# Kernel tuning notes

Hardware: AMD Instinct MI355X
Metric: run time of the kernel (lower is better)

The kernel has to match this reference:

```python
import jax, jax.numpy as jnp
import numpy as np

N = 50000      # nodes
E = 1600000    # edges
F_IN = 128     # input_dim
H = 160        # hidden_dim
G = 512        # graphs in batch
C = 2          # num_classes
EPS = 1e-5     # BatchNorm eps


def setup_inputs() -> dict:
    key = jax.random.key(0)
    ks = jax.random.split(key, 12)
    x = jax.random.normal(ks[0], (N, F_IN), jnp.float32)
    edge_index = jax.random.randint(ks[1], (2, E), 0, N, dtype=jnp.int32)
    batch = jnp.sort(jax.random.randint(ks[2], (N,), 0, G, dtype=jnp.int32))

    def lin(k, fi, fo):
        s = 1.0 / np.sqrt(fi)
        kw, kb = jax.random.split(k)
        W = jax.random.uniform(kw, (fi, fo), jnp.float32, -s, s)
        b = jax.random.uniform(kb, (fo,), jnp.float32, -s, s)
        return W, b

    W1, b1 = lin(ks[3], F_IN, H)
    W2, b2 = lin(ks[4], H, H)
    W3, b3 = lin(ks[5], H, H)
    Wc1, bc1 = lin(ks[6], H, H // 2)
    Wc2, bc2 = lin(ks[7], H // 2, C)

    def bn(k):
        k1, k2, k3, k4 = jax.random.split(k, 4)
        gamma = jax.random.uniform(k1, (H,), jnp.float32, 0.5, 1.5)
        beta = jax.random.normal(k2, (H,), jnp.float32) * 0.1
        mean = jax.random.normal(k3, (H,), jnp.float32) * 0.1
        var = jax.random.uniform(k4, (H,), jnp.float32, 0.5, 1.5)
        return gamma, beta, mean, var

    g1, be1, m1, v1 = bn(ks[8])
    g2, be2, m2, v2 = bn(ks[9])
    g3, be3, m3, v3 = bn(ks[10])

    return dict(x=x, edge_index=edge_index, batch=batch,
                W1=W1, b1=b1, W2=W2, b2=b2, W3=W3, b3=b3,
                g1=g1, be1=be1, m1=m1, v1=v1,
                g2=g2, be2=be2, m2=m2, v2=v2,
                g3=g3, be3=be3, m3=m3, v3=v3,
                Wc1=Wc1, bc1=bc1, Wc2=Wc2, bc2=bc2)


def gcn_conv(x, W, b, src, dst):
    """PyG GCNConv: symmetric deg normalization with self-loops; lin -> aggregate -> +bias."""
    n = x.shape[0]
    h = x @ W                                   # [N, H]
    loop = jnp.arange(n, dtype=src.dtype)
    s = jnp.concatenate([src, loop])            # self-loops appended
    d = jnp.concatenate([dst, loop])
    deg = jax.ops.segment_sum(jnp.ones_like(d, jnp.float32), d, num_segments=n)
    inv = jnp.where(deg > 0, jax.lax.rsqrt(deg), 0.0)
    msg = h[s] * (inv[s] * inv[d])[:, None]     # [E+N, H] gather + norm
    return jax.ops.segment_sum(msg, d, num_segments=n) + b


def bn_eval(x, gamma, beta, mean, var):
    return (x - mean) * jax.lax.rsqrt(var + EPS) * gamma + beta


def reference(x, edge_index, batch, W1, b1, W2, b2, W3, b3,
              g1, be1, m1, v1, g2, be2, m2, v2, g3, be3, m3, v3,
              Wc1, bc1, Wc2, bc2):
    src, dst = edge_index[0], edge_index[1]
    # eval mode: dropout is identity, BN uses running stats
    h = jax.nn.relu(bn_eval(gcn_conv(x, W1, b1, src, dst), g1, be1, m1, v1))
    h = jax.nn.relu(bn_eval(gcn_conv(h, W2, b2, src, dst), g2, be2, m2, v2))
    h = jax.nn.relu(bn_eval(gcn_conv(h, W3, b3, src, dst), g3, be3, m3, v3))
    # global mean pool over graph ids
    sums = jax.ops.segment_sum(h, batch, num_segments=G)
    cnt = jax.ops.segment_sum(jnp.ones((h.shape[0],), jnp.float32), batch, num_segments=G)
    pooled = sums / jnp.clip(cnt, 1.0)[:, None]
    # MLP head
    z = jax.nn.relu(pooled @ Wc1 + bc1)
    return z @ Wc2 + bc2
```

## Files before the change

### kernel.cpp

```cpp
#include <hip/hip_runtime.h>

#define N_NODES   50000
#define N_EDGES   1600000
#define FDIM_IN   128
#define HDIM      160
#define N_GRAPHS  512
#define BN_EPS    1e-5f
#define NBKT_MAX  256
#define BKT_SH    8
#define HIST_BLOCKS 128

typedef _Float16 h2   __attribute__((ext_vector_type(2)));
typedef _Float16 f16x8 __attribute__((ext_vector_type(8)));
typedef float  facc4 __attribute__((ext_vector_type(4)));


__device__ __forceinline__ unsigned short f2h_bits(float f) {
    union { _Float16 h; unsigned short s; } c;
    c.h = (_Float16)f;
    return c.s;
}

__device__ __forceinline__ unsigned int pkh(float lo, float hi) {
    return (unsigned int)f2h_bits(lo) | ((unsigned int)f2h_bits(hi) << 16);
}

__device__ __forceinline__ h2 u2h(unsigned int u) {
    union { unsigned int u; h2 h; } c; c.u = u; return c.h;
}

__device__ __forceinline__ unsigned int h2u(h2 h) {
    union { unsigned int u; h2 h; } c; c.h = h; return c.u;
}

__device__ __forceinline__ void addpk16(h2* acc, uint4 r) {
    acc[0] += u2h(r.x);
    acc[1] += u2h(r.y);
    acc[2] += u2h(r.z);
    acc[3] += u2h(r.w);
}


__global__ __launch_bounds__(256) void coarse_hist_kernel(const int* __restrict__ dst,
                                                          int* __restrict__ cg, int E) {
    __shared__ int h[NBKT_MAX];
    int tid = threadIdx.x;
    if (tid < NBKT_MAX) h[tid] = 0;
    __syncthreads();
    for (int e = blockIdx.x * 256 + tid; e < E; e += gridDim.x * 256)
        atomicAdd(&h[dst[e] >> BKT_SH], 1);
    __syncthreads();
    if (tid < NBKT_MAX) cg[blockIdx.x * NBKT_MAX + tid] = h[tid];
}


struct PrepArgs {
    const float *b, *g, *be, *m, *v;
    float *sc, *sh;
};

__global__ __launch_bounds__(256) void setup_kernel(const int* __restrict__ cg,
                                                    int* __restrict__ bucket_base,
                                                    int* __restrict__ bucket_cursor,
                                                    PrepArgs a0, PrepArgs a1, PrepArgs a2,
                                                    const float* __restrict__ W1,
                                                    const float* __restrict__ W2,
                                                    const float* __restrict__ W3,
                                                    unsigned short* __restrict__ o1,
                                                    unsigned short* __restrict__ o2,
                                                    unsigned short* __restrict__ o3) {
    int bid = blockIdx.x;
    int t = threadIdx.x;
    if (bid == 0) {
        __shared__ int h[NBKT_MAX];
        __shared__ int total;
        if (t < NBKT_MAX) {
            int s = 0;
            for (int b = 0; b < HIST_BLOCKS; ++b) s += cg[b * NBKT_MAX + t];
            h[t] = s;
        }
        __syncthreads();
        if (t == 0) {
            int run = 0;
            for (int i = 0; i < NBKT_MAX; ++i) { int c = h[i]; h[i] = run; run += c; }
            total = run;
        }
        __syncthreads();
        if (t < NBKT_MAX) {
            bucket_base[t] = h[t];
            bucket_cursor[t] = h[t];
        }
        if (t == 0) bucket_base[NBKT_MAX] = total;
    } else if (bid <= 3) {
        PrepArgs a = (bid == 1) ? a0 : (bid == 2) ? a1 : a2;
        if (t < HDIM) {
            float s = a.g[t] * rsqrtf(a.v[t] + BN_EPS);
            a.sc[t] = s;
            a.sh[t] = (a.b[t] - a.m[t]) * s + a.be[t];
        }
    } else {
        int i = (bid - 4) * 256 + t;
        const float* W;
        unsigned short* o;
        if (i < 128 * 160)                 { W = W1; o = o1; }
        else if (i < 128 * 160 + 160 * 160) { W = W2; o = o2; i -= 128 * 160; }
        else if (i < 128 * 160 + 2 * 160 * 160) { W = W3; o = o3; i -= 128 * 160 + 160 * 160; }
        else return;
        int j = i & 7;
        int l = (i >> 3) & 63;
        int u = (i >> 9) % 10;
        int tt = i / 5120;
        int k = tt * 32 + (l >> 4) * 8 + j;
        int nn = u * 16 + (l & 15);
        o[i] = f2h_bits(W[k * 160 + nn]);
    }
}

__global__ __launch_bounds__(256) void part_kernel(const int* __restrict__ src,
                                                   const int* __restrict__ dst,
                                                   int* __restrict__ bucket_cursor,
                                                   unsigned int* __restrict__ pairs, int E) {
    __shared__ int bcnt[NBKT_MAX], bbase[NBKT_MAX], lc[NBKT_MAX];
    int tid = threadIdx.x;
    int per = (E + gridDim.x - 1) / gridDim.x;
    int beg = blockIdx.x * per;
    int end = min(beg + per, E);
    if (tid < NBKT_MAX) { bcnt[tid] = 0; lc[tid] = 0; }
    __syncthreads();
    for (int e = beg + tid; e < end; e += 256)
        atomicAdd(&bcnt[dst[e] >> BKT_SH], 1);
    __syncthreads();
    if (tid < NBKT_MAX)
        bbase[tid] = bcnt[tid] ? atomicAdd(&bucket_cursor[tid], bcnt[tid]) : 0;
    __syncthreads();
    for (int e = beg + tid; e < end; e += 256) {
        int d = dst[e];
        int b = d >> BKT_SH;
        int pos = bbase[b] + atomicAdd(&lc[b], 1);
        pairs[pos] = ((unsigned int)src[e] << BKT_SH) | (unsigned int)(d & (NBKT_MAX - 1));
    }
}

__global__ __launch_bounds__(1024) void bucket_csr_kernel(const unsigned int* __restrict__ pairs,
                                                          const int* __restrict__ bucket_base,
                                                          int* __restrict__ row_off,
                                                          float* __restrict__ inv,
                                                          int* __restrict__ ssrc,
                                                          const float* __restrict__ x,
                                                          unsigned short* __restrict__ xs,
                                                          int n) {
    __shared__ int h[NBKT_MAX];
    __shared__ int ws[4];
    __shared__ float sinv[NBKT_MAX];
    int tid = threadIdx.x;
    int b = blockIdx.x;
    int node0 = b << BKT_SH;
    int beg = bucket_base[b], end = bucket_base[b + 1];
    if (tid < NBKT_MAX) h[tid] = 0;
    __syncthreads();
    for (int j = beg + tid; j < end; j += 1024)
        atomicAdd(&h[pairs[j] & (NBKT_MAX - 1)], 1);
    __syncthreads();
    int cntv = (tid < NBKT_MAX) ? h[tid] : 0;
    __syncthreads();
    int lane = tid & 63, wid = tid >> 6;
    int incl = cntv;
    #pragma unroll
    for (int off = 1; off < 64; off <<= 1) {
        int u = __shfl_up(incl, off);
        if (lane >= off) incl += u;
    }
    if (tid < NBKT_MAX && lane == 63) ws[wid] = incl;
    __syncthreads();
    if (tid == 0) {
        int r = 0;
        #pragma unroll
        for (int i = 0; i < 4; ++i) { int t = ws[i]; ws[i] = r; r += t; }
    }
    __syncthreads();
    int excl = (tid < NBKT_MAX) ? (ws[wid] + incl - cntv) : 0;
    if (tid < NBKT_MAX) {
        float iv = rsqrtf((float)(cntv + 1));
        int node = node0 + tid;
        if (node < n) {
            row_off[node] = beg + excl;
            inv[node] = iv;
        }
        sinv[tid] = iv;
        h[tid] = excl;
    }
    if (tid == 0 && (node0 + NBKT_MAX) >= n) row_off[n] = end;
    __syncthreads();
    for (int j = beg + tid; j < end; j += 1024) {
        unsigned int p = pairs[j];
        int pos = beg + atomicAdd(&h[p & (NBKT_MAX - 1)], 1);
        ssrc[pos] = (int)(p >> BKT_SH);
    }
    for (int idx = tid; idx < NBKT_MAX * 32; idx += 1024) {
        int nd = node0 + (idx >> 5);
        if (nd < n) {
            float w = sinv[idx >> 5];
            float4 v = ((const float4*)x)[(size_t)nd * 32 + (idx & 31)];
            ushort4 o;
            o.x = f2h_bits(v.x * w); o.y = f2h_bits(v.y * w);
            o.z = f2h_bits(v.z * w); o.w = f2h_bits(v.w * w);
            ((ushort4*)xs)[(size_t)nd * 32 + (idx & 31)] = o;
        }
    }
}


template <int C>
__global__ __launch_bounds__(256) void agg_grp_kernel(const unsigned short* __restrict__ in_s,
                                                      const float* __restrict__ inv,
                                                      const int* __restrict__ row_off,
                                                      const int* __restrict__ ssrc,
                                                      unsigned short* __restrict__ out,
                                                      int base, int n) {
    constexpr int LPR = C / 8;
    constexpr int G   = 64 / LPR;
    constexpr int RB  = C * 2;
    int wave = threadIdx.x >> 6;
    int lane = threadIdx.x & 63;
    int node = base + blockIdx.x * 4 + wave;
    if (node >= n) return;
    int g  = lane / LPR;
    int cl = lane - g * LPR;
    bool act = g < G;
    int beg = row_off[node], end = row_off[node + 1];
    const char* bptr = (const char*)in_s;
    int lb = cl * 16;

    h2 acc[4];
    #pragma unroll
    for (int i = 0; i < 4; ++i) acc[i] = (h2){(_Float16)0.f, (_Float16)0.f};

    if (g == 0) {
        uint4 r = *(const uint4*)(bptr + (size_t)node * RB + lb);
        addpk16(acc, r);
    }

    int e = act ? beg + g : end;
    for (; e + G < end; e += 2 * G) {
        int s0 = ssrc[e], s1 = ssrc[e + G];
        uint4 r0 = *(const uint4*)(bptr + (size_t)s0 * RB + lb);
        uint4 r1 = *(const uint4*)(bptr + (size_t)s1 * RB + lb);
        addpk16(acc, r0);
        addpk16(acc, r1);
    }
    if (e < end) {
        uint4 r = *(const uint4*)(bptr + (size_t)ssrc[e] * RB + lb);
        addpk16(acc, r);
    }

    if (G == 4) {
        #pragma unroll
        for (int i = 0; i < 4; ++i) acc[i] += u2h(__shfl(h2u(acc[i]), lane + 32));
        #pragma unroll
        for (int i = 0; i < 4; ++i) acc[i] += u2h(__shfl(h2u(acc[i]), lane + 16));
    } else {
        #pragma unroll
        for (int i = 0; i < 4; ++i) {
            unsigned int ua = __shfl(h2u(acc[i]), lane + 20);
            unsigned int ub = __shfl(h2u(acc[i]), lane + 40);
            acc[i] += u2h(ua) + u2h(ub);
        }
    }

    if (lane < LPR) {
        float wi = inv[node];
        uint4 o;
        o.x = pkh((float)acc[0].x * wi, (float)acc[0].y * wi);
        o.y = pkh((float)acc[1].x * wi, (float)acc[1].y * wi);
        o.z = pkh((float)acc[2].x * wi, (float)acc[2].y * wi);
        o.w = pkh((float)acc[3].x * wi, (float)acc[3].y * wi);
        *(uint4*)((char*)out + (size_t)node * RB + lb) = o;
    }
}


template <int K, int OUTMODE>
__global__ __launch_bounds__(256) void mfma_gemm_kernel(const unsigned short* __restrict__ A,
                                                        const unsigned short* __restrict__ Bp,
                                                        const float* __restrict__ sc,
                                                        const float* __restrict__ sh,
                                                        const float* __restrict__ inv,
                                                        float* __restrict__ CoutF,
                                                        unsigned short* __restrict__ CoutB,
                                                        int n) {
    constexpr int KT = K / 32;
    constexpr int BQ = K * 20;
    __shared__ uint4 Bs[BQ];
    int tid = threadIdx.x;
    for (int i = tid; i < BQ; i += 256) Bs[i] = ((const uint4*)Bp)[i];

    int wave = tid >> 6, lane = tid & 63;
    int m = lane & 15, q = lane >> 4;
    int row0 = blockIdx.x * 128 + wave * 16;
    int row1 = row0 + 64;

    int ar0 = row0 + m; ar0 = (ar0 < n) ? ar0 : (n - 1);
    int ar1 = row1 + m; ar1 = (ar1 < n) ? ar1 : (n - 1);
    const f16x8* A0 = (const f16x8*)(A + (size_t)ar0 * K);
    const f16x8* A1 = (const f16x8*)(A + (size_t)ar1 * K);
    const f16x8* Bf = (const f16x8*)Bs;

    facc4 acc0[10], acc1[10];
    #pragma unroll
    for (int u = 0; u < 10; ++u) {
        acc0[u] = (facc4){0.f, 0.f, 0.f, 0.f};
        acc1[u] = (facc4){0.f, 0.f, 0.f, 0.f};
    }

    __syncthreads();

    #pragma unroll
    for (int t = 0; t < KT; ++t) {
        f16x8 af0 = A0[t * 4 + q];
        f16x8 af1 = A1[t * 4 + q];
        #pragma unroll
        for (int u = 0; u < 10; ++u) {
            f16x8 bf = Bf[(t * 10 + u) * 64 + lane];
            acc0[u] = __builtin_amdgcn_mfma_f32_16x16x32_f16(af0, bf, acc0[u], 0, 0, 0);
            acc1[u] = __builtin_amdgcn_mfma_f32_16x16x32_f16(af1, bf, acc1[u], 0, 0, 0);
        }
    }

    #pragma unroll
    for (int u = 0; u < 10; ++u) {
        int c = u * 16 + m;
        float scv = sc[c], shv = sh[c];
        #pragma unroll
        for (int r = 0; r < 4; ++r) {
            int rr = row0 + q * 4 + r;
            if (rr < n) {
                float v = fmaxf(acc0[u][r] * scv + shv, 0.f);
                if (OUTMODE == 1) CoutB[(size_t)rr * 160 + c] = f2h_bits(v * inv[rr]);
                else              CoutF[(size_t)rr * 160 + c] = v;
            }
            int rr1 = row1 + q * 4 + r;
            if (rr1 < n) {
                float v = fmaxf(acc1[u][r] * scv + shv, 0.f);
                if (OUTMODE == 1) CoutB[(size_t)rr1 * 160 + c] = f2h_bits(v * inv[rr1]);
                else              CoutF[(size_t)rr1 * 160 + c] = v;
            }
        }
    }
}


__global__ __launch_bounds__(256) void pool_head_kernel(const float* __restrict__ h,
                                                        const int* __restrict__ batch,
                                                        const float* __restrict__ Wc1,
                                                        const float* __restrict__ bc1,
                                                        const float* __restrict__ Wc2,
                                                        const float* __restrict__ bc2,
                                                        float* __restrict__ out, int n) {
    __shared__ float4 part[6][40];
    __shared__ float pooled[160];
    __shared__ float z[80];
    __shared__ int range[2];
    int g = blockIdx.x;
    int t = threadIdx.x;
    if (t < 2) {
        int target = g + t;
        int lo = 0, hi = n;
        while (lo < hi) {
            int mid = (lo + hi) >> 1;
            if (batch[mid] < target) lo = mid + 1; else hi = mid;
        }
        range[t] = lo;
    }
    __syncthreads();
    int lo = range[0], hi = range[1];
    int sub = t / 40, c4 = t - sub * 40;
    if (sub < 6) {
        float4 a = {0.f, 0.f, 0.f, 0.f};
        for (int r = lo + sub; r < hi; r += 6) {
            float4 v = ((const float4*)(h + (size_t)r * 160))[c4];
            a.x += v.x; a.y += v.y; a.z += v.z; a.w += v.w;
        }
        part[sub][c4] = a;
    }
    __syncthreads();
    if (t < 40) {
        float4 s = {0.f, 0.f, 0.f, 0.f};
        #pragma unroll
        for (int i = 0; i < 6; ++i) {
            float4 p = part[i][t];
            s.x += p.x; s.y += p.y; s.z += p.z; s.w += p.w;
        }
        float ic = 1.f / fmaxf((float)(hi - lo), 1.f);
        pooled[t * 4 + 0] = s.x * ic;
        pooled[t * 4 + 1] = s.y * ic;
        pooled[t * 4 + 2] = s.z * ic;
        pooled[t * 4 + 3] = s.w * ic;
    }
    __syncthreads();
    if (t < 80) {
        float s = bc1[t];
        for (int k = 0; k < 160; ++k) s += pooled[k] * Wc1[k * 80 + t];
        z[t] = fmaxf(s, 0.f);
    }
    __syncthreads();
    if (t < 2) {
        float s = bc2[t];
        for (int k = 0; k < 80; ++k) s += z[k] * Wc2[k * 2 + t];
        out[g * 2 + t] = s;
    }
}


static inline size_t align256(size_t x) { return (x + 255) & ~(size_t)255; }

extern "C" void kernel_launch(void* const* d_in, const int* in_sizes, int n_in,
                              void* d_out, int out_size, void* d_ws, size_t ws_size,
                              hipStream_t stream) {
    const float* x   = (const float*)d_in[0];
    const int* ei    = (const int*)d_in[1];
    const int* batch = (const int*)d_in[2];
    const float* W1  = (const float*)d_in[3];
    const float* b1  = (const float*)d_in[4];
    const float* W2  = (const float*)d_in[5];
    const float* b2  = (const float*)d_in[6];
    const float* W3  = (const float*)d_in[7];
    const float* b3  = (const float*)d_in[8];
    const float* g1  = (const float*)d_in[9];
    const float* be1 = (const float*)d_in[10];
    const float* m1  = (const float*)d_in[11];
    const float* v1  = (const float*)d_in[12];
    const float* g2  = (const float*)d_in[13];
    const float* be2 = (const float*)d_in[14];
    const float* m2  = (const float*)d_in[15];
    const float* v2  = (const float*)d_in[16];
    const float* g3  = (const float*)d_in[17];
    const float* be3 = (const float*)d_in[18];
    const float* m3  = (const float*)d_in[19];
    const float* v3  = (const float*)d_in[20];
    const float* Wc1 = (const float*)d_in[21];
    const float* bc1 = (const float*)d_in[22];
    const float* Wc2 = (const float*)d_in[23];
    const float* bc2 = (const float*)d_in[24];
    float* out = (float*)d_out;

    const int N = in_sizes[2];
    const int E = in_sizes[1] / 2;
    const int* src = ei;
    const int* dst = ei + E;

    char* w = (char*)d_ws;
    int*   row_off = (int*)w;             w += align256((size_t)(N + 1) * 4);
    float* inv     = (float*)w;           w += align256((size_t)N * 4);
    int*   ssrc    = (int*)w;             w += align256((size_t)E * 4);
    unsigned int* pairs = (unsigned int*)w; w += align256((size_t)E * 4);
    int*   cg      = (int*)w;             w += align256((size_t)HIST_BLOCKS * NBKT_MAX * 4);
    int*   bucket_base   = (int*)w;       w += align256((size_t)(NBKT_MAX + 1) * 4);
    int*   bucket_cursor = (int*)w;       w += align256((size_t)NBKT_MAX * 4);
    float* scsh    = (float*)w;           w += align256((size_t)6 * HDIM * 4);
    unsigned short* W1p = (unsigned short*)w;  w += align256((size_t)FDIM_IN * HDIM * 2);
    unsigned short* W2p = (unsigned short*)w;  w += align256((size_t)HDIM * HDIM * 2);
    unsigned short* W3p = (unsigned short*)w;  w += align256((size_t)HDIM * HDIM * 2);
    unsigned short* bufA_bf = (unsigned short*)w;  w += align256((size_t)N * HDIM * 2);
    char* regionR = w;
    unsigned short* xs_bf = (unsigned short*)regionR;
    unsigned short* hs_bf = (unsigned short*)(regionR + align256((size_t)N * FDIM_IN * 2));
    float* bufB = (float*)regionR;
    float* sc1 = scsh, *sh1 = scsh + 160, *sc2 = scsh + 320, *sh2 = scsh + 480,
         * sc3 = scsh + 640, *sh3 = scsh + 800;

    coarse_hist_kernel<<<HIST_BLOCKS, 256, 0, stream>>>(dst, cg, E);

    PrepArgs pa0 = {b1, g1, be1, m1, v1, sc1, sh1};
    PrepArgs pa1 = {b2, g2, be2, m2, v2, sc2, sh2};
    PrepArgs pa2 = {b3, g3, be3, m3, v3, sc3, sh3};
    int packTotal = 128 * 160 + 2 * 160 * 160;
    int setupBlocks = 4 + (packTotal + 255) / 256;
    setup_kernel<<<setupBlocks, 256, 0, stream>>>(cg, bucket_base, bucket_cursor,
                                                  pa0, pa1, pa2, W1, W2, W3, W1p, W2p, W3p);

    part_kernel<<<256, 256, 0, stream>>>(src, dst, bucket_cursor, pairs, E);
    int nbkt = (N + NBKT_MAX - 1) >> BKT_SH;
    bucket_csr_kernel<<<nbkt, 1024, 0, stream>>>(pairs, bucket_base, row_off, inv, ssrc, x, xs_bf, N);

    int half = ((N / 2) + 3) & ~3;
    int gA1 = half / 4;
    int gA2 = (N - half + 3) / 4;
    int gGemm = (N + 127) / 128;

    agg_grp_kernel<128><<<gA1, 256, 0, stream>>>(xs_bf, inv, row_off, ssrc, bufA_bf, 0, half);
    agg_grp_kernel<128><<<gA2, 256, 0, stream>>>(xs_bf, inv, row_off, ssrc, bufA_bf, half, N);
    mfma_gemm_kernel<128, 1><<<gGemm, 256, 0, stream>>>(bufA_bf, W1p, sc1, sh1, inv, nullptr, hs_bf, N);
    agg_grp_kernel<160><<<gA1, 256, 0, stream>>>(hs_bf, inv, row_off, ssrc, bufA_bf, 0, half);
    agg_grp_kernel<160><<<gA2, 256, 0, stream>>>(hs_bf, inv, row_off, ssrc, bufA_bf, half, N);
    mfma_gemm_kernel<160, 1><<<gGemm, 256, 0, stream>>>(bufA_bf, W2p, sc2, sh2, inv, nullptr, hs_bf, N);
    agg_grp_kernel<160><<<gA1, 256, 0, stream>>>(hs_bf, inv, row_off, ssrc, bufA_bf, 0, half);
    agg_grp_kernel<160><<<gA2, 256, 0, stream>>>(hs_bf, inv, row_off, ssrc, bufA_bf, half, N);
    mfma_gemm_kernel<160, 0><<<gGemm, 256, 0, stream>>>(bufA_bf, W3p, sc3, sh3, inv, bufB, nullptr, N);

    pool_head_kernel<<<N_GRAPHS, 256, 0, stream>>>(bufB, batch, Wc1, bc1, Wc2, bc2, out, N);
}
```

Before: 480.0 us.

## Fuse neighbor aggregation with MFMA GEMM per 16-node tile in one kernel

Replaces the separate aggregation kernels and GEMM kernel per layer with one fused kernel. A single wave aggregates 16 nodes into LDS, then runs MFMA against the packed weights read directly from global memory. This removes the intermediate aggregated-buffer write and read and two launches per layer, and unrolls the gather loop by four. The trade-off is that one wave handles 16 nodes serially with little latency hiding, weights are re-read from global or cache by each block, and the buffers no longer alias.

```diff
diff --git a/kernel.cpp b/kernel.cpp
--- a/kernel.cpp
+++ b/kernel.cpp
@@ -210,119 +210,109 @@
 }
 
 
-template <int C>
-__global__ __launch_bounds__(256) void agg_grp_kernel(const unsigned short* __restrict__ in_s,
-                                                      const float* __restrict__ inv,
-                                                      const int* __restrict__ row_off,
-                                                      const int* __restrict__ ssrc,
-                                                      unsigned short* __restrict__ out,
-                                                      int base, int n) {
-    constexpr int LPR = C / 8;
+template <int CIN, int OUTMODE>
+__global__ __launch_bounds__(64) void fused_layer_kernel(const unsigned short* __restrict__ in_s,
+                                                         const float* __restrict__ inv,
+                                                         const int* __restrict__ row_off,
+                                                         const int* __restrict__ ssrc,
+                                                         const unsigned short* __restrict__ Bp,
+                                                         const float* __restrict__ sc,
+                                                         const float* __restrict__ sh,
+                                                         float* __restrict__ CoutF,
+                                                         unsigned short* __restrict__ CoutB,
+                                                         int n) {
+    constexpr int LPR = CIN / 8;
     constexpr int G   = 64 / LPR;
-    constexpr int RB  = C * 2;
-    int wave = threadIdx.x >> 6;
-    int lane = threadIdx.x & 63;
-    int node = base + blockIdx.x * 4 + wave;
-    if (node >= n) return;
+    constexpr int RB  = CIN * 2;
+    constexpr int KT  = CIN / 32;
+    constexpr int STR = CIN + 8;
+    __shared__ unsigned short hrow[16][STR];
+
+    int lane = threadIdx.x;
+    int node0 = blockIdx.x * 16;
     int g  = lane / LPR;
     int cl = lane - g * LPR;
     bool act = g < G;
-    int beg = row_off[node], end = row_off[node + 1];
+    int lb = cl * 16;
     const char* bptr = (const char*)in_s;
-    int lb = cl * 16;
-
-    h2 acc[4];
+
+    for (int i = 0; i < 16; ++i) {
+        int node = node0 + i;
+        if (node >= n) break;
+        int beg = row_off[node], end = row_off[node + 1];
+
+        h2 acc[4];
+        #pragma unroll
+        for (int k = 0; k < 4; ++k) acc[k] = (h2){(_Float16)0.f, (_Float16)0.f};
+
+        if (g == 0) {
+            uint4 r = *(const uint4*)(bptr + (size_t)node * RB + lb);
+            addpk16(acc, r);
+        }
+
+        int e = act ? beg + g : end;
+        for (; e + 3 * G < end; e += 4 * G) {
+            int s0 = ssrc[e],         s1 = ssrc[e + G];
+            int s2 = ssrc[e + 2 * G], s3 = ssrc[e + 3 * G];
+            uint4 r0 = *(const uint4*)(bptr + (size_t)s0 * RB + lb);
+            uint4 r1 = *(const uint4*)(bptr + (size_t)s1 * RB + lb);
+            uint4 r2 = *(const uint4*)(bptr + (size_t)s2 * RB + lb);
+            uint4 r3 = *(const uint4*)(bptr + (size_t)s3 * RB + lb);
+            addpk16(acc, r0); addpk16(acc, r1);
+            addpk16(acc, r2); addpk16(acc, r3);
+        }
+        if (e + G < end) {
+            int s0 = ssrc[e], s1 = ssrc[e + G];
+            uint4 r0 = *(const uint4*)(bptr + (size_t)s0 * RB + lb);
+            uint4 r1 = *(const uint4*)(bptr + (size_t)s1 * RB + lb);
+            addpk16(acc, r0); addpk16(acc, r1);
+            e += 2 * G;
+        }
+        if (e < end) {
+            uint4 r = *(const uint4*)(bptr + (size_t)ssrc[e] * RB + lb);
+            addpk16(acc, r);
+        }
+
+        if (G == 4) {
+            #pragma unroll
+            for (int k = 0; k < 4; ++k) acc[k] += u2h(__shfl(h2u(acc[k]), lane + 32));
+            #pragma unroll
+            for (int k = 0; k < 4; ++k) acc[k] += u2h(__shfl(h2u(acc[k]), lane + 16));
+        } else {
+            #pragma unroll
+            for (int k = 0; k < 4; ++k) {
+                unsigned int ua = __shfl(h2u(acc[k]), lane + 20);
+                unsigned int ub = __shfl(h2u(acc[k]), lane + 40);
+                acc[k] += u2h(ua) + u2h(ub);
+            }
+        }
+
+        if (lane < LPR) {
+            float wi = inv[node];
+            uint4 o;
+            o.x = pkh((float)acc[0].x * wi, (float)acc[0].y * wi);
+            o.y = pkh((float)acc[1].x * wi, (float)acc[1].y * wi);
+            o.z = pkh((float)acc[2].x * wi, (float)acc[2].y * wi);
+            o.w = pkh((float)acc[3].x * wi, (float)acc[3].y * wi);
+            *(uint4*)&hrow[i][cl * 8] = o;
+        }
+    }
+    __syncthreads();
+
+    int m = lane & 15, q = lane >> 4;
+    const f16x8* Bf = (const f16x8*)Bp;
+
+    facc4 acc[10];
     #pragma unroll
-    for (int i = 0; i < 4; ++i) acc[i] = (h2){(_Float16)0.f, (_Float16)0.f};
-
-    if (g == 0) {
-        uint4 r = *(const uint4*)(bptr + (size_t)node * RB + lb);
-        addpk16(acc, r);
-    }
-
-    int e = act ? beg + g : end;
-    for (; e + G < end; e += 2 * G) {
-        int s0 = ssrc[e], s1 = ssrc[e + G];
-        uint4 r0 = *(const uint4*)(bptr + (size_t)s0 * RB + lb);
-        uint4 r1 = *(const uint4*)(bptr + (size_t)s1 * RB + lb);
-        addpk16(acc, r0);
-        addpk16(acc, r1);
-    }
-    if (e < end) {
-        uint4 r = *(const uint4*)(bptr + (size_t)ssrc[e] * RB + lb);
-        addpk16(acc, r);
-    }
-
-    if (G == 4) {
-        #pragma unroll
-        for (int i = 0; i < 4; ++i) acc[i] += u2h(__shfl(h2u(acc[i]), lane + 32));
-        #pragma unroll
-        for (int i = 0; i < 4; ++i) acc[i] += u2h(__shfl(h2u(acc[i]), lane + 16));
-    } else {
-        #pragma unroll
-        for (int i = 0; i < 4; ++i) {
-            unsigned int ua = __shfl(h2u(acc[i]), lane + 20);
-            unsigned int ub = __shfl(h2u(acc[i]), lane + 40);
-            acc[i] += u2h(ua) + u2h(ub);
-        }
-    }
-
-    if (lane < LPR) {
-        float wi = inv[node];
-        uint4 o;
-        o.x = pkh((float)acc[0].x * wi, (float)acc[0].y * wi);
-        o.y = pkh((float)acc[1].x * wi, (float)acc[1].y * wi);
-        o.z = pkh((float)acc[2].x * wi, (float)acc[2].y * wi);
-        o.w = pkh((float)acc[3].x * wi, (float)acc[3].y * wi);
-        *(uint4*)((char*)out + (size_t)node * RB + lb) = o;
-    }
-}
-
-
-template <int K, int OUTMODE>
-__global__ __launch_bounds__(256) void mfma_gemm_kernel(const unsigned short* __restrict__ A,
-                                                        const unsigned short* __restrict__ Bp,
-                                                        const float* __restrict__ sc,
-                                                        const float* __restrict__ sh,
-                                                        const float* __restrict__ inv,
-                                                        float* __restrict__ CoutF,
-                                                        unsigned short* __restrict__ CoutB,
-                                                        int n) {
-    constexpr int KT = K / 32;
-    constexpr int BQ = K * 20;
-    __shared__ uint4 Bs[BQ];
-    int tid = threadIdx.x;
-    for (int i = tid; i < BQ; i += 256) Bs[i] = ((const uint4*)Bp)[i];
-
-    int wave = tid >> 6, lane = tid & 63;
-    int m = lane & 15, q = lane >> 4;
-    int row0 = blockIdx.x * 128 + wave * 16;
-    int row1 = row0 + 64;
-
-    int ar0 = row0 + m; ar0 = (ar0 < n) ? ar0 : (n - 1);
-    int ar1 = row1 + m; ar1 = (ar1 < n) ? ar1 : (n - 1);
-    const f16x8* A0 = (const f16x8*)(A + (size_t)ar0 * K);
-    const f16x8* A1 = (const f16x8*)(A + (size_t)ar1 * K);
-    const f16x8* Bf = (const f16x8*)Bs;
-
-    facc4 acc0[10], acc1[10];
-    #pragma unroll
-    for (int u = 0; u < 10; ++u) {
-        acc0[u] = (facc4){0.f, 0.f, 0.f, 0.f};
-        acc1[u] = (facc4){0.f, 0.f, 0.f, 0.f};
-    }
-
-    __syncthreads();
+    for (int u = 0; u < 10; ++u) acc[u] = (facc4){0.f, 0.f, 0.f, 0.f};
 
     #pragma unroll
     for (int t = 0; t < KT; ++t) {
-        f16x8 af0 = A0[t * 4 + q];
-        f16x8 af1 = A1[t * 4 + q];
+        f16x8 af = *(const f16x8*)&hrow[m][t * 32 + q * 8];
         #pragma unroll
         for (int u = 0; u < 10; ++u) {
             f16x8 bf = Bf[(t * 10 + u) * 64 + lane];
-            acc0[u] = __builtin_amdgcn_mfma_f32_16x16x32_f16(af0, bf, acc0[u], 0, 0, 0);
-            acc1[u] = __builtin_amdgcn_mfma_f32_16x16x32_f16(af1, bf, acc1[u], 0, 0, 0);
+            acc[u] = __builtin_amdgcn_mfma_f32_16x16x32_f16(af, bf, acc[u], 0, 0, 0);
         }
     }
 
@@ -332,17 +322,11 @@
         float scv = sc[c], shv = sh[c];
         #pragma unroll
         for (int r = 0; r < 4; ++r) {
-            int rr = row0 + q * 4 + r;
+            int rr = node0 + q * 4 + r;
             if (rr < n) {
-                float v = fmaxf(acc0[u][r] * scv + shv, 0.f);
+                float v = fmaxf(acc[u][r] * scv + shv, 0.f);
                 if (OUTMODE == 1) CoutB[(size_t)rr * 160 + c] = f2h_bits(v * inv[rr]);
                 else              CoutF[(size_t)rr * 160 + c] = v;
-            }
-            int rr1 = row1 + q * 4 + r;
-            if (rr1 < n) {
-                float v = fmaxf(acc1[u][r] * scv + shv, 0.f);
-                if (OUTMODE == 1) CoutB[(size_t)rr1 * 160 + c] = f2h_bits(v * inv[rr1]);
-                else              CoutF[(size_t)rr1 * 160 + c] = v;
             }
         }
     }
@@ -460,11 +444,10 @@
     unsigned short* W1p = (unsigned short*)w;  w += align256((size_t)FDIM_IN * HDIM * 2);
     unsigned short* W2p = (unsigned short*)w;  w += align256((size_t)HDIM * HDIM * 2);
     unsigned short* W3p = (unsigned short*)w;  w += align256((size_t)HDIM * HDIM * 2);
-    unsigned short* bufA_bf = (unsigned short*)w;  w += align256((size_t)N * HDIM * 2);
-    char* regionR = w;
-    unsigned short* xs_bf = (unsigned short*)regionR;
-    unsigned short* hs_bf = (unsigned short*)(regionR + align256((size_t)N * FDIM_IN * 2));
-    float* bufB = (float*)regionR;
+    unsigned short* xs_bf  = (unsigned short*)w;  w += align256((size_t)N * FDIM_IN * 2);
+    unsigned short* h1_bf  = (unsigned short*)w;  w += align256((size_t)N * HDIM * 2);
+    unsigned short* h2_bf  = (unsigned short*)w;  w += align256((size_t)N * HDIM * 2);
+    float* bufC    = (float*)w;           w += align256((size_t)N * HDIM * 4);
     float* sc1 = scsh, *sh1 = scsh + 160, *sc2 = scsh + 320, *sh2 = scsh + 480,
          * sc3 = scsh + 640, *sh3 = scsh + 800;
 
@@ -482,20 +465,11 @@
     int nbkt = (N + NBKT_MAX - 1) >> BKT_SH;
     bucket_csr_kernel<<<nbkt, 1024, 0, stream>>>(pairs, bucket_base, row_off, inv, ssrc, x, xs_bf, N);
 
-    int half = ((N / 2) + 3) & ~3;
-    int gA1 = half / 4;
-    int gA2 = (N - half + 3) / 4;
-    int gGemm = (N + 127) / 128;
-
-    agg_grp_kernel<128><<<gA1, 256, 0, stream>>>(xs_bf, inv, row_off, ssrc, bufA_bf, 0, half);
-    agg_grp_kernel<128><<<gA2, 256, 0, stream>>>(xs_bf, inv, row_off, ssrc, bufA_bf, half, N);
-    mfma_gemm_kernel<128, 1><<<gGemm, 256, 0, stream>>>(bufA_bf, W1p, sc1, sh1, inv, nullptr, hs_bf, N);
-    agg_grp_kernel<160><<<gA1, 256, 0, stream>>>(hs_bf, inv, row_off, ssrc, bufA_bf, 0, half);
-    agg_grp_kernel<160><<<gA2, 256, 0, stream>>>(hs_bf, inv, row_off, ssrc, bufA_bf, half, N);
-    mfma_gemm_kernel<160, 1><<<gGemm, 256, 0, stream>>>(bufA_bf, W2p, sc2, sh2, inv, nullptr, hs_bf, N);
-    agg_grp_kernel<160><<<gA1, 256, 0, stream>>>(hs_bf, inv, row_off, ssrc, bufA_bf, 0, half);
-    agg_grp_kernel<160><<<gA2, 256, 0, stream>>>(hs_bf, inv, row_off, ssrc, bufA_bf, half, N);
-    mfma_gemm_kernel<160, 0><<<gGemm, 256, 0, stream>>>(bufA_bf, W3p, sc3, sh3, inv, bufB, nullptr, N);
-
-    pool_head_kernel<<<N_GRAPHS, 256, 0, stream>>>(bufB, batch, Wc1, bc1, Wc2, bc2, out, N);
-}
+    int gF = (N + 15) / 16;
+
+    fused_layer_kernel<128, 1><<<gF, 64, 0, stream>>>(xs_bf, inv, row_off, ssrc, W1p, sc1, sh1, nullptr, h1_bf, N);
+    fused_layer_kernel<160, 1><<<gF, 64, 0, stream>>>(h1_bf, inv, row_off, ssrc, W2p, sc2, sh2, nullptr, h2_bf, N);
+    fused_layer_kernel<160, 0><<<gF, 64, 0, stream>>>(h2_bf, inv, row_off, ssrc, W3p, sc3, sh3, bufC, nullptr, N);
+
+    pool_head_kernel<<<N_GRAPHS, 256, 0, stream>>>(bufC, batch, Wc1, bc1, Wc2, bc2, out, N);
+}
```

Result: faster. 427.5 us (-10.9%).
